# Kernel tuning notes

Measured on AMD Instinct MI355X. Metric: run time of the kernel, lower is better.

## Reference

```python
import jax, jax.numpy as jnp
import numpy as np

HEADS = 24
KV_HEADS = 6
HEAD_DIM = 64


def _partial_rope(x, cos, sin):
    # x: [B, H, S, head_dim]; cos/sin: [S, rot_dim]; rotate first rot_dim dims
    rot_dim = cos.shape[-1]
    x_rot, x_pass = x[..., :rot_dim], x[..., rot_dim:]
    half = rot_dim // 2
    # use_real_unbind_dim=-2: reshape (..., 2, half) then unbind -> first/second half
    x_real, x_imag = x_rot[..., :half], x_rot[..., half:]
    x_rotated = jnp.concatenate([-x_imag, x_real], axis=-1)
    out = x_rot * cos[None, None] + x_rotated * sin[None, None]
    return jnp.concatenate([out, x_pass], axis=-1)


def setup_inputs() -> dict:
    key = jax.random.key(0)
    ks = jax.random.split(key, 8)
    B, S, D = 2, 2048, 1536
    kv_dim = KV_HEADS * HEAD_DIM
    rot_dim = 32
    hidden_states = jax.random.normal(ks[0], (B, S, D), dtype=jnp.float32)
    # realistic rotary cos/sin from inv-freq angles
    pos = jnp.arange(S, dtype=jnp.float32)
    inv_freq = 1.0 / (10000.0 ** (jnp.arange(0, rot_dim, 2, dtype=jnp.float32) / rot_dim))
    ang = pos[:, None] * inv_freq[None, :]  # [S, rot_dim//2]
    ang = jnp.concatenate([ang, ang], axis=-1)  # [S, rot_dim]
    cos, sin = jnp.cos(ang), jnp.sin(ang)
    Wq = jax.random.normal(ks[1], (D, D), dtype=jnp.float32) * 0.02
    Wk = jax.random.normal(ks[2], (D, kv_dim), dtype=jnp.float32) * 0.02
    Wv = jax.random.normal(ks[3], (D, kv_dim), dtype=jnp.float32) * 0.02
    Wo = jax.random.normal(ks[4], (D, D), dtype=jnp.float32) * 0.02
    bo = jnp.zeros((D,), dtype=jnp.float32)
    return {"hidden_states": hidden_states, "cos": cos, "sin": sin,
            "Wq": Wq, "Wk": Wk, "Wv": Wv, "Wo": Wo, "bo": bo}


def reference(hidden_states, cos, sin, Wq, Wk, Wv, Wo, bo):
    B, S, D = hidden_states.shape
    residual = hidden_states
    q = hidden_states @ Wq  # [B,S,D]
    k = hidden_states @ Wk  # [B,S,kv_dim]
    v = hidden_states @ Wv
    q = q.reshape(B, S, HEADS, HEAD_DIM).transpose(0, 2, 1, 3)       # [B,H,S,d]
    k = k.reshape(B, S, KV_HEADS, HEAD_DIM).transpose(0, 2, 1, 3)    # [B,Hkv,S,d]
    v = v.reshape(B, S, KV_HEADS, HEAD_DIM).transpose(0, 2, 1, 3)
    rep = HEADS // KV_HEADS
    k = jnp.repeat(k, rep, axis=1)  # GQA repeat_interleave -> [B,H,S,d]
    v = jnp.repeat(v, rep, axis=1)
    # partial RoPE on query and key (self-attention)
    q = _partial_rope(q, cos, sin)
    k = _partial_rope(k, cos, sin)
    scale = 1.0 / jnp.sqrt(jnp.float32(HEAD_DIM))
    scores = jnp.einsum('bhqd,bhkd->bhqk', q, k) * scale
    probs = jax.nn.softmax(scores, axis=-1)
    out = jnp.einsum('bhqk,bhkd->bhqd', probs, v)
    out = out.transpose(0, 2, 1, 3).reshape(B, S, D)
    out = out @ Wo + bo
    return out + residual
```

## Files before the change

### kernel.cpp

```cpp
#include <hip/hip_runtime.h>

#define HEADS 24
#define KVH   6
#define HD    64
#define BB    2
#define SS    2048
#define DD    1536
#define KVD   384
#define NTOT  2304
#define MM    4096

typedef unsigned short ushort_t;
typedef __attribute__((ext_vector_type(8))) short short8;
typedef __attribute__((ext_vector_type(4))) float f32x4;

__device__ __forceinline__ ushort_t f2bf(float f) {
    union { float f; unsigned u; } v; v.f = f;
    return (ushort_t)((v.u + 0x8000u) >> 16);
}
__device__ __forceinline__ ushort_t f2bf_trunc(float f) {
    union { float f; unsigned u; } v; v.f = f;
    return (ushort_t)(v.u >> 16);
}
__device__ __forceinline__ unsigned pk2(float a, float b) {
    union { float f; unsigned u; } x, y; x.f = a; y.f = b;
    return ((x.u + 0x8000u) >> 16) | (((y.u + 0x8000u) >> 16) << 16);
}
#if __has_builtin(__builtin_amdgcn_exp2f)
#define EXP2(x) __builtin_amdgcn_exp2f(x)
#else
#define EXP2(x) exp2f(x)
#endif
__device__ __forceinline__ void glds16(const void* g, void* l) {
    __builtin_amdgcn_global_load_lds(
        (const __attribute__((address_space(1))) void*)g,
        (__attribute__((address_space(3))) void*)l, 16, 0, 0);
}

__device__ __forceinline__ void tconv_body(const float* __restrict__ in,
                                           ushort_t* __restrict__ out,
                                           int R, int C, int cb, int rb)
{
    __shared__ ushort_t tile[32][33];
    const int tx = threadIdx.x & 31, ty = threadIdx.x >> 5;
    const int c0 = cb * 32, r0 = rb * 32;
#pragma unroll
    for (int i = 0; i < 4; ++i)
        tile[ty + i * 8][tx] = f2bf(in[(size_t)(r0 + ty + i * 8) * C + c0 + tx]);
    __syncthreads();
#pragma unroll
    for (int i = 0; i < 4; ++i)
        out[(size_t)(c0 + ty + i * 8) * R + r0 + tx] = tile[tx][ty + i * 8];
}

#define NCVT (MM * DD / 4 / 256)
__global__ __launch_bounds__(256) void k_prep(const float* __restrict__ HS,
                                              const float* __restrict__ Wq,
                                              const float* __restrict__ Wk,
                                              const float* __restrict__ Wv,
                                              const float* __restrict__ Wo,
                                              ushort_t* __restrict__ Xbf,
                                              ushort_t* __restrict__ Wqt,
                                              ushort_t* __restrict__ Wkt,
                                              ushort_t* __restrict__ Wvt,
                                              ushort_t* __restrict__ Wot)
{
    int bid = blockIdx.x;
    if (bid < NCVT) {
        int i = bid * 256 + threadIdx.x;
        float4 v = ((const float4*)HS)[i];
        uint2 o = { pk2(v.x, v.y), pk2(v.z, v.w) };
        ((uint2*)Xbf)[i] = o;
        return;
    }
    bid -= NCVT;
    if (bid < 2304) { tconv_body(Wq, Wqt, DD, DD,  bid % 48, bid / 48); return; }
    bid -= 2304;
    if (bid < 576)  { tconv_body(Wk, Wkt, DD, KVD, bid % 12, bid / 12); return; }
    bid -= 576;
    if (bid < 576)  { tconv_body(Wv, Wvt, DD, KVD, bid % 12, bid / 12); return; }
    bid -= 576;
    tconv_body(Wo, Wot, DD, DD, bid % 48, bid / 48);
}

__global__ __launch_bounds__(256) void k_vt(const ushort_t* __restrict__ QKVb,
                                            ushort_t* __restrict__ VT)
{
    __shared__ ushort_t tile[32][33];
    const int tx = threadIdx.x & 31, ty = threadIdx.x >> 5;
    const int s0 = blockIdx.x * 32, c0 = blockIdx.y * 32, b = blockIdx.z;
#pragma unroll
    for (int i = 0; i < 4; ++i)
        tile[ty + i * 8][tx] =
            QKVb[(size_t)(b * SS + s0 + ty + i * 8) * NTOT + DD + KVD + c0 + tx];
    __syncthreads();
#pragma unroll
    for (int i = 0; i < 4; ++i)
        VT[((size_t)b * KVD + c0 + ty + i * 8) * SS + s0 + tx] = tile[tx][ty + i * 8];
}

__global__ __launch_bounds__(256) void k_qkv_mfma(const ushort_t* __restrict__ Xbf,
                                                  const ushort_t* __restrict__ Wqt,
                                                  const ushort_t* __restrict__ Wkt,
                                                  const ushort_t* __restrict__ Wvt,
                                                  const float* __restrict__ cosb,
                                                  const float* __restrict__ sinb,
                                                  ushort_t* __restrict__ QKVb)
{
    __shared__ ushort_t As[128][32];
    __shared__ ushort_t Bs[128][32];
    const int t = threadIdx.x, lane = t & 63, wave = t >> 6;
    const int n16 = lane & 15, quad = lane >> 4;
    const int wr = wave >> 1, wc = wave & 1;
    const int nt = blockIdx.x;
    const int n0 = nt * 128;
    const int m0 = blockIdx.y * 128;
    const ushort_t* Bt; int nl, mode;
    if (nt < 12)      { Bt = Wqt; nl = n0;            mode = 0; }
    else if (nt < 15) { Bt = Wkt; nl = n0 - DD;       mode = 1; }
    else              { Bt = Wvt; nl = n0 - DD - KVD; mode = 2; }

    const int srow = lane >> 2;
    const int scol = (lane & 3) * 8;
    const size_t aoff0 = (size_t)(m0 + wave * 16 + srow) * DD + scol;
    const size_t aoff1 = (size_t)(m0 + (wave + 4) * 16 + srow) * DD + scol;
    const size_t boff0 = (size_t)(nl + wave * 16 + srow) * DD + scol;
    const size_t boff1 = (size_t)(nl + (wave + 4) * 16 + srow) * DD + scol;
    ushort_t* lA0 = &As[wave * 16][0];
    ushort_t* lA1 = &As[(wave + 4) * 16][0];
    ushort_t* lB0 = &Bs[wave * 16][0];
    ushort_t* lB1 = &Bs[(wave + 4) * 16][0];

    f32x4 acc[4][4] = {};
    for (int k0 = 0; k0 < DD; k0 += 32) {
        __syncthreads();
        glds16(Xbf + aoff0 + k0, lA0);
        glds16(Xbf + aoff1 + k0, lA1);
        glds16(Bt  + boff0 + k0, lB0);
        glds16(Bt  + boff1 + k0, lB1);
        __syncthreads();
        short8 af[4], bf8[4];
#pragma unroll
        for (int i = 0; i < 4; ++i) af[i]  = *(const short8*)&As[wr * 64 + i * 16 + n16][quad * 8];
#pragma unroll
        for (int j = 0; j < 4; ++j) bf8[j] = *(const short8*)&Bs[wc * 64 + j * 16 + n16][quad * 8];
#pragma unroll
        for (int i = 0; i < 4; ++i)
#pragma unroll
            for (int j = 0; j < 4; ++j)
                acc[i][j] = __builtin_amdgcn_mfma_f32_16x16x32_bf16(af[i], bf8[j], acc[i][j], 0, 0, 0);
    }

    const float QSC = 0.18033688011112042f;
#pragma unroll
    for (int i = 0; i < 4; ++i) {
#pragma unroll
        for (int r = 0; r < 4; ++r) {
            const int row = m0 + wr * 64 + i * 16 + quad * 4 + r;
            ushort_t* outp = QKVb + (size_t)row * NTOT + n0 + wc * 64 + n16;
            float v0 = acc[i][0][r], v1 = acc[i][1][r];
            float v2 = acc[i][2][r], v3 = acc[i][3][r];
            if (mode < 2) {
                const int s = row & (SS - 1);
                float c0 = cosb[s * 32 + n16],      s0 = sinb[s * 32 + n16];
                float c1 = cosb[s * 32 + 16 + n16], s1 = sinb[s * 32 + 16 + n16];
                float nr = v0 * c0 - v1 * s0;
                float ni = v1 * c1 + v0 * s1;
                v0 = nr; v1 = ni;
            }
            if (mode == 0) { v0 *= QSC; v1 *= QSC; v2 *= QSC; v3 *= QSC; }
            outp[0]  = f2bf(v0);
            outp[16] = f2bf(v1);
            outp[32] = f2bf(v2);
            outp[48] = f2bf(v3);
        }
    }
}

__global__ __launch_bounds__(256) void k_attn(const ushort_t* __restrict__ QKVb,
                                              const ushort_t* __restrict__ VT,
                                              ushort_t* __restrict__ AOb)
{
    __shared__ __align__(16) ushort_t Ks[64][72];
    __shared__ __align__(16) ushort_t Vs[64][72];
    __shared__ __align__(16) ushort_t Ps[128][76];

    const int t    = threadIdx.x;
    const int wave = t >> 6;
    const int quad = (t >> 4) & 3;
    const int n16  = t & 15;
    const int q0   = blockIdx.x * 128;
    const int h    = blockIdx.y;
    const int b    = blockIdx.z;
    const int kh   = h >> 2;

    const int sr = t >> 2;
    const int sc = (t & 3) * 8;
    const int vc = (t & 3) * 16;

    short8 qf[2][2];
#pragma unroll
    for (int m = 0; m < 2; ++m)
#pragma unroll
        for (int kc = 0; kc < 2; ++kc)
            qf[m][kc] = *(const short8*)(QKVb +
                (size_t)(b * SS + q0 + wave * 32 + m * 16 + n16) * NTOT +
                h * HD + kc * 32 + quad * 8);

    float l_p[2][4] = {};
    f32x4 acc_o[2][4] = {};

    const ushort_t* Kbase = QKVb + (size_t)(b * SS) * NTOT + DD + kh * HD;
    const ushort_t* Vbase = VT + ((size_t)b * KVD + kh * 64) * SS;

    uint4 kp0, kp1, vp0, vp1;
    {
        const ushort_t* Kg = Kbase + (size_t)sr * NTOT + sc;
        kp0 = *(const uint4*)(Kg);
        kp1 = *(const uint4*)(Kg + 32);
        const ushort_t* Vg = Vbase + (size_t)sr * SS + vc;
        vp0 = *(const uint4*)(Vg);
        vp1 = *(const uint4*)(Vg + 8);
    }

    for (int kt = 0; kt < SS / 64; ++kt) {
        __syncthreads();
        *(uint4*)&Ks[sr][sc]      = kp0;
        *(uint4*)&Ks[sr][sc + 32] = kp1;
        *(uint4*)&Vs[sr][vc]      = vp0;
        *(uint4*)&Vs[sr][vc + 8]  = vp1;
        __syncthreads();

        if (kt + 1 < SS / 64) {
            const int k0n = (kt + 1) * 64;
            const ushort_t* Kg = Kbase + (size_t)(k0n + sr) * NTOT + sc;
            kp0 = *(const uint4*)(Kg);
            kp1 = *(const uint4*)(Kg + 32);
            const ushort_t* Vg = Vbase + (size_t)sr * SS + k0n + vc;
            vp0 = *(const uint4*)(Vg);
            vp1 = *(const uint4*)(Vg + 8);
        }

        f32x4 s_acc[2][4] = {};
#pragma unroll
        for (int kc = 0; kc < 2; ++kc) {
            short8 bf[4];
#pragma unroll
            for (int jj = 0; jj < 4; ++jj)
                bf[jj] = *(const short8*)&Ks[jj * 16 + n16][kc * 32 + quad * 8];
#pragma unroll
            for (int m = 0; m < 2; ++m)
#pragma unroll
                for (int jj = 0; jj < 4; ++jj)
                    s_acc[m][jj] = __builtin_amdgcn_mfma_f32_16x16x32_bf16(
                        qf[m][kc], bf[jj], s_acc[m][jj], 0, 0, 0);
        }

#pragma unroll
        for (int m = 0; m < 2; ++m)
#pragma unroll
            for (int r = 0; r < 4; ++r) {
                float p0 = EXP2(s_acc[m][0][r]);
                float p1 = EXP2(s_acc[m][1][r]);
                float p2 = EXP2(s_acc[m][2][r]);
                float p3 = EXP2(s_acc[m][3][r]);
                ushort_t* pr = &Ps[wave * 32 + m * 16 + quad * 4 + r][n16];
                pr[0]  = f2bf_trunc(p0);
                pr[16] = f2bf_trunc(p1);
                pr[32] = f2bf_trunc(p2);
                pr[48] = f2bf_trunc(p3);
                l_p[m][r] += (p0 + p1) + (p2 + p3);
            }

#pragma unroll
        for (int kc = 0; kc < 2; ++kc) {
            short8 vb[4];
#pragma unroll
            for (int dd = 0; dd < 4; ++dd)
                vb[dd] = *(const short8*)&Vs[dd * 16 + n16][kc * 32 + quad * 8];
#pragma unroll
            for (int m = 0; m < 2; ++m) {
                short8 pa = *(const short8*)&Ps[wave * 32 + m * 16 + n16][kc * 32 + quad * 8];
#pragma unroll
                for (int dd = 0; dd < 4; ++dd)
                    acc_o[m][dd] = __builtin_amdgcn_mfma_f32_16x16x32_bf16(
                        pa, vb[dd], acc_o[m][dd], 0, 0, 0);
            }
        }
    }

#pragma unroll
    for (int m = 0; m < 2; ++m) {
        float inv[4];
#pragma unroll
        for (int r = 0; r < 4; ++r) {
            float s = l_p[m][r];
#pragma unroll
            for (int msk = 1; msk < 16; msk <<= 1)
                s += __shfl_xor(s, msk);
            inv[r] = 1.0f / s;
        }
#pragma unroll
        for (int dd = 0; dd < 4; ++dd)
#pragma unroll
            for (int r = 0; r < 4; ++r) {
                int q = q0 + wave * 32 + m * 16 + quad * 4 + r;
                AOb[(size_t)(b * SS + q) * DD + h * HD + dd * 16 + n16] =
                    f2bf(acc_o[m][dd][r] * inv[r]);
            }
    }
}

__global__ __launch_bounds__(256) void k_out_mfma(const ushort_t* __restrict__ AOb,
                                                  const ushort_t* __restrict__ Wot,
                                                  const float* __restrict__ bo,
                                                  const float* __restrict__ HS,
                                                  float* __restrict__ out)
{
    __shared__ ushort_t As[128][32];
    __shared__ ushort_t Bs[128][32];
    const int t = threadIdx.x, lane = t & 63, wave = t >> 6;
    const int n16 = lane & 15, quad = lane >> 4;
    const int wr = wave >> 1, wc = wave & 1;
    const int n0 = blockIdx.x * 128;
    const int m0 = blockIdx.y * 128;

    const int srow = lane >> 2;
    const int scol = (lane & 3) * 8;
    const size_t aoff0 = (size_t)(m0 + wave * 16 + srow) * DD + scol;
    const size_t aoff1 = (size_t)(m0 + (wave + 4) * 16 + srow) * DD + scol;
    const size_t boff0 = (size_t)(n0 + wave * 16 + srow) * DD + scol;
    const size_t boff1 = (size_t)(n0 + (wave + 4) * 16 + srow) * DD + scol;
    ushort_t* lA0 = &As[wave * 16][0];
    ushort_t* lA1 = &As[(wave + 4) * 16][0];
    ushort_t* lB0 = &Bs[wave * 16][0];
    ushort_t* lB1 = &Bs[(wave + 4) * 16][0];

    f32x4 acc[4][4] = {};
    for (int k0 = 0; k0 < DD; k0 += 32) {
        __syncthreads();
        glds16(AOb + aoff0 + k0, lA0);
        glds16(AOb + aoff1 + k0, lA1);
        glds16(Wot + boff0 + k0, lB0);
        glds16(Wot + boff1 + k0, lB1);
        __syncthreads();
        short8 af[4], bf8[4];
#pragma unroll
        for (int i = 0; i < 4; ++i) af[i]  = *(const short8*)&As[wr * 64 + i * 16 + n16][quad * 8];
#pragma unroll
        for (int j = 0; j < 4; ++j) bf8[j] = *(const short8*)&Bs[wc * 64 + j * 16 + n16][quad * 8];
#pragma unroll
        for (int i = 0; i < 4; ++i)
#pragma unroll
            for (int j = 0; j < 4; ++j)
                acc[i][j] = __builtin_amdgcn_mfma_f32_16x16x32_bf16(af[i], bf8[j], acc[i][j], 0, 0, 0);
    }

    const int colb = n0 + wc * 64 + n16;
    float bo4[4];
#pragma unroll
    for (int j = 0; j < 4; ++j) bo4[j] = bo[colb + j * 16];
#pragma unroll
    for (int i = 0; i < 4; ++i) {
#pragma unroll
        for (int r = 0; r < 4; ++r) {
            const int row = m0 + wr * 64 + i * 16 + quad * 4 + r;
            float* op = out + (size_t)row * DD + colb;
            const float* hp = HS + (size_t)row * DD + colb;
#pragma unroll
            for (int j = 0; j < 4; ++j)
                op[j * 16] = acc[i][j][r] + bo4[j] + hp[j * 16];
        }
    }
}

extern "C" void kernel_launch(void* const* d_in, const int* in_sizes, int n_in,
                              void* d_out, int out_size, void* d_ws, size_t ws_size,
                              hipStream_t stream)
{
    const float* HS   = (const float*)d_in[0];
    const float* cosb = (const float*)d_in[1];
    const float* sinb = (const float*)d_in[2];
    const float* Wq   = (const float*)d_in[3];
    const float* Wk   = (const float*)d_in[4];
    const float* Wv   = (const float*)d_in[5];
    const float* Wo   = (const float*)d_in[6];
    const float* bo   = (const float*)d_in[7];
    float* out = (float*)d_out;

    ushort_t* Xbf  = (ushort_t*)d_ws;
    ushort_t* QKVb = Xbf  + (size_t)MM * DD;
    ushort_t* AOb  = QKVb + (size_t)MM * NTOT;
    ushort_t* Wqt  = AOb  + (size_t)MM * DD;
    ushort_t* Wkt  = Wqt  + (size_t)DD * DD;
    ushort_t* Wvt  = Wkt  + (size_t)KVD * DD;
    ushort_t* Wot  = Wvt  + (size_t)KVD * DD;
    ushort_t* VT   = Wot  + (size_t)DD * DD;

    const int nprep = NCVT + 2304 + 576 + 576 + 2304;
    k_prep    <<<dim3(nprep), 256, 0, stream>>>(HS, Wq, Wk, Wv, Wo,
                                                Xbf, Wqt, Wkt, Wvt, Wot);
    k_qkv_mfma<<<dim3(NTOT / 128, MM / 128), 256, 0, stream>>>(Xbf, Wqt, Wkt, Wvt, cosb, sinb, QKVb);
    k_vt      <<<dim3(SS / 32, KVD / 32, BB), 256, 0, stream>>>(QKVb, VT);
    k_attn    <<<dim3(SS / 128, HEADS, BB),   256, 0, stream>>>(QKVb, VT, AOb);
    k_out_mfma<<<dim3(DD / 128, MM / 128),    256, 0, stream>>>(AOb, Wot, bo, HS, out);
}
```

Before: 309.0 us.

## Compute V transposed directly via dedicated GEMM, drop transpose kernel

The V projection moves out of the fused QKV GEMM into a new kernel that computes Wv^T·X^T, so V is written already transposed and the separate k_vt transpose pass with its QKV round trip is removed. The QKV buffer shrinks to Q and K only. The output projection tile is halved in M (64x128) to launch more blocks. The attention K/V register prefetch is removed in favour of direct global-to-LDS loads each iteration, which may expose more load latency.

```diff
diff --git a/kernel.cpp b/kernel.cpp
--- a/kernel.cpp
+++ b/kernel.cpp
@@ -7,7 +7,7 @@
 #define SS    2048
 #define DD    1536
 #define KVD   384
-#define NTOT  2304
+#define QKD   1920
 #define MM    4096
 
 typedef unsigned short ushort_t;
@@ -83,26 +83,9 @@
     tconv_body(Wo, Wot, DD, DD, bid % 48, bid / 48);
 }
 
-__global__ __launch_bounds__(256) void k_vt(const ushort_t* __restrict__ QKVb,
-                                            ushort_t* __restrict__ VT)
-{
-    __shared__ ushort_t tile[32][33];
-    const int tx = threadIdx.x & 31, ty = threadIdx.x >> 5;
-    const int s0 = blockIdx.x * 32, c0 = blockIdx.y * 32, b = blockIdx.z;
-#pragma unroll
-    for (int i = 0; i < 4; ++i)
-        tile[ty + i * 8][tx] =
-            QKVb[(size_t)(b * SS + s0 + ty + i * 8) * NTOT + DD + KVD + c0 + tx];
-    __syncthreads();
-#pragma unroll
-    for (int i = 0; i < 4; ++i)
-        VT[((size_t)b * KVD + c0 + ty + i * 8) * SS + s0 + tx] = tile[tx][ty + i * 8];
-}
-
 __global__ __launch_bounds__(256) void k_qkv_mfma(const ushort_t* __restrict__ Xbf,
                                                   const ushort_t* __restrict__ Wqt,
                                                   const ushort_t* __restrict__ Wkt,
-                                                  const ushort_t* __restrict__ Wvt,
                                                   const float* __restrict__ cosb,
                                                   const float* __restrict__ sinb,
                                                   ushort_t* __restrict__ QKVb)
@@ -115,10 +98,9 @@
     const int nt = blockIdx.x;
     const int n0 = nt * 128;
     const int m0 = blockIdx.y * 128;
-    const ushort_t* Bt; int nl, mode;
-    if (nt < 12)      { Bt = Wqt; nl = n0;            mode = 0; }
-    else if (nt < 15) { Bt = Wkt; nl = n0 - DD;       mode = 1; }
-    else              { Bt = Wvt; nl = n0 - DD - KVD; mode = 2; }
+    const ushort_t* Bt; int nl, isq;
+    if (nt < 12) { Bt = Wqt; nl = n0;      isq = 1; }
+    else         { Bt = Wkt; nl = n0 - DD; isq = 0; }
 
     const int srow = lane >> 2;
     const int scol = (lane & 3) * 8;
@@ -157,10 +139,10 @@
 #pragma unroll
         for (int r = 0; r < 4; ++r) {
             const int row = m0 + wr * 64 + i * 16 + quad * 4 + r;
-            ushort_t* outp = QKVb + (size_t)row * NTOT + n0 + wc * 64 + n16;
+            ushort_t* outp = QKVb + (size_t)row * QKD + n0 + wc * 64 + n16;
             float v0 = acc[i][0][r], v1 = acc[i][1][r];
             float v2 = acc[i][2][r], v3 = acc[i][3][r];
-            if (mode < 2) {
+            {
                 const int s = row & (SS - 1);
                 float c0 = cosb[s * 32 + n16],      s0 = sinb[s * 32 + n16];
                 float c1 = cosb[s * 32 + 16 + n16], s1 = sinb[s * 32 + 16 + n16];
@@ -168,13 +150,66 @@
                 float ni = v1 * c1 + v0 * s1;
                 v0 = nr; v1 = ni;
             }
-            if (mode == 0) { v0 *= QSC; v1 *= QSC; v2 *= QSC; v3 *= QSC; }
+            if (isq) { v0 *= QSC; v1 *= QSC; v2 *= QSC; v3 *= QSC; }
             outp[0]  = f2bf(v0);
             outp[16] = f2bf(v1);
             outp[32] = f2bf(v2);
             outp[48] = f2bf(v3);
         }
     }
+}
+
+__global__ __launch_bounds__(256) void k_vtg(const ushort_t* __restrict__ Wvt,
+                                             const ushort_t* __restrict__ Xbf,
+                                             ushort_t* __restrict__ VT)
+{
+    __shared__ ushort_t As[64][32];
+    __shared__ ushort_t Bs[128][32];
+    const int t = threadIdx.x, lane = t & 63, wave = t >> 6;
+    const int n16 = lane & 15, quad = lane >> 4;
+    const int wr = wave >> 1, wc = wave & 1;
+    const int n0 = blockIdx.x * 128;
+    const int m0 = blockIdx.y * 64;
+
+    const int srow = lane >> 2;
+    const int scol = (lane & 3) * 8;
+    const size_t aoff  = (size_t)(m0 + wave * 16 + srow) * DD + scol;
+    const size_t boff0 = (size_t)(n0 + wave * 32 + srow) * DD + scol;
+    const size_t boff1 = boff0 + (size_t)16 * DD;
+    ushort_t* lA  = &As[wave * 16][0];
+    ushort_t* lB0 = &Bs[wave * 32][0];
+    ushort_t* lB1 = &Bs[wave * 32 + 16][0];
+
+    f32x4 acc[2][4] = {};
+    for (int k0 = 0; k0 < DD; k0 += 32) {
+        __syncthreads();
+        glds16(Wvt + aoff  + k0, lA);
+        glds16(Xbf + boff0 + k0, lB0);
+        glds16(Xbf + boff1 + k0, lB1);
+        __syncthreads();
+        short8 af[2], bf8[4];
+#pragma unroll
+        for (int i = 0; i < 2; ++i) af[i]  = *(const short8*)&As[wr * 32 + i * 16 + n16][quad * 8];
+#pragma unroll
+        for (int j = 0; j < 4; ++j) bf8[j] = *(const short8*)&Bs[wc * 64 + j * 16 + n16][quad * 8];
+#pragma unroll
+        for (int i = 0; i < 2; ++i)
+#pragma unroll
+            for (int j = 0; j < 4; ++j)
+                acc[i][j] = __builtin_amdgcn_mfma_f32_16x16x32_bf16(af[i], bf8[j], acc[i][j], 0, 0, 0);
+    }
+
+    const int b = n0 >> 11;
+#pragma unroll
+    for (int i = 0; i < 2; ++i)
+#pragma unroll
+        for (int r = 0; r < 4; ++r) {
+            const int c = m0 + wr * 32 + i * 16 + quad * 4 + r;
+            ushort_t* op = VT + ((size_t)b * KVD + c) * SS + (n0 & (SS - 1)) + wc * 64 + n16;
+#pragma unroll
+            for (int j = 0; j < 4; ++j)
+                op[j * 16] = f2bf(acc[i][j][r]);
+        }
 }
 
 __global__ __launch_bounds__(256) void k_attn(const ushort_t* __restrict__ QKVb,
@@ -204,42 +239,27 @@
 #pragma unroll
         for (int kc = 0; kc < 2; ++kc)
             qf[m][kc] = *(const short8*)(QKVb +
-                (size_t)(b * SS + q0 + wave * 32 + m * 16 + n16) * NTOT +
+                (size_t)(b * SS + q0 + wave * 32 + m * 16 + n16) * QKD +
                 h * HD + kc * 32 + quad * 8);
 
     float l_p[2][4] = {};
     f32x4 acc_o[2][4] = {};
 
-    const ushort_t* Kbase = QKVb + (size_t)(b * SS) * NTOT + DD + kh * HD;
+    const ushort_t* Kbase = QKVb + (size_t)(b * SS) * QKD + DD + kh * HD;
     const ushort_t* Vbase = VT + ((size_t)b * KVD + kh * 64) * SS;
 
-    uint4 kp0, kp1, vp0, vp1;
-    {
-        const ushort_t* Kg = Kbase + (size_t)sr * NTOT + sc;
-        kp0 = *(const uint4*)(Kg);
-        kp1 = *(const uint4*)(Kg + 32);
-        const ushort_t* Vg = Vbase + (size_t)sr * SS + vc;
-        vp0 = *(const uint4*)(Vg);
-        vp1 = *(const uint4*)(Vg + 8);
-    }
-
     for (int kt = 0; kt < SS / 64; ++kt) {
-        __syncthreads();
-        *(uint4*)&Ks[sr][sc]      = kp0;
-        *(uint4*)&Ks[sr][sc + 32] = kp1;
-        *(uint4*)&Vs[sr][vc]      = vp0;
-        *(uint4*)&Vs[sr][vc + 8]  = vp1;
-        __syncthreads();
-
-        if (kt + 1 < SS / 64) {
-            const int k0n = (kt + 1) * 64;
-            const ushort_t* Kg = Kbase + (size_t)(k0n + sr) * NTOT + sc;
-            kp0 = *(const uint4*)(Kg);
-            kp1 = *(const uint4*)(Kg + 32);
-            const ushort_t* Vg = Vbase + (size_t)sr * SS + k0n + vc;
-            vp0 = *(const uint4*)(Vg);
-            vp1 = *(const uint4*)(Vg + 8);
-        }
+        const int k0 = kt * 64;
+        __syncthreads();
+        {
+            const ushort_t* Kg = Kbase + (size_t)(k0 + sr) * QKD + sc;
+            *(uint4*)&Ks[sr][sc]      = *(const uint4*)(Kg);
+            *(uint4*)&Ks[sr][sc + 32] = *(const uint4*)(Kg + 32);
+            const ushort_t* Vg = Vbase + (size_t)sr * SS + k0 + vc;
+            *(uint4*)&Vs[sr][vc]      = *(const uint4*)(Vg);
+            *(uint4*)&Vs[sr][vc + 8]  = *(const uint4*)(Vg + 8);
+        }
+        __syncthreads();
 
         f32x4 s_acc[2][4] = {};
 #pragma unroll
@@ -317,40 +337,37 @@
                                                   const float* __restrict__ HS,
                                                   float* __restrict__ out)
 {
-    __shared__ ushort_t As[128][32];
+    __shared__ ushort_t As[64][32];
     __shared__ ushort_t Bs[128][32];
     const int t = threadIdx.x, lane = t & 63, wave = t >> 6;
     const int n16 = lane & 15, quad = lane >> 4;
     const int wr = wave >> 1, wc = wave & 1;
     const int n0 = blockIdx.x * 128;
-    const int m0 = blockIdx.y * 128;
+    const int m0 = blockIdx.y * 64;
 
     const int srow = lane >> 2;
     const int scol = (lane & 3) * 8;
-    const size_t aoff0 = (size_t)(m0 + wave * 16 + srow) * DD + scol;
-    const size_t aoff1 = (size_t)(m0 + (wave + 4) * 16 + srow) * DD + scol;
-    const size_t boff0 = (size_t)(n0 + wave * 16 + srow) * DD + scol;
-    const size_t boff1 = (size_t)(n0 + (wave + 4) * 16 + srow) * DD + scol;
-    ushort_t* lA0 = &As[wave * 16][0];
-    ushort_t* lA1 = &As[(wave + 4) * 16][0];
-    ushort_t* lB0 = &Bs[wave * 16][0];
-    ushort_t* lB1 = &Bs[(wave + 4) * 16][0];
-
-    f32x4 acc[4][4] = {};
+    const size_t aoff  = (size_t)(m0 + wave * 16 + srow) * DD + scol;
+    const size_t boff0 = (size_t)(n0 + wave * 32 + srow) * DD + scol;
+    const size_t boff1 = boff0 + (size_t)16 * DD;
+    ushort_t* lA  = &As[wave * 16][0];
+    ushort_t* lB0 = &Bs[wave * 32][0];
+    ushort_t* lB1 = &Bs[wave * 32 + 16][0];
+
+    f32x4 acc[2][4] = {};
     for (int k0 = 0; k0 < DD; k0 += 32) {
         __syncthreads();
-        glds16(AOb + aoff0 + k0, lA0);
-        glds16(AOb + aoff1 + k0, lA1);
+        glds16(AOb + aoff  + k0, lA);
         glds16(Wot + boff0 + k0, lB0);
         glds16(Wot + boff1 + k0, lB1);
         __syncthreads();
-        short8 af[4], bf8[4];
-#pragma unroll
-        for (int i = 0; i < 4; ++i) af[i]  = *(const short8*)&As[wr * 64 + i * 16 + n16][quad * 8];
+        short8 af[2], bf8[4];
+#pragma unroll
+        for (int i = 0; i < 2; ++i) af[i]  = *(const short8*)&As[wr * 32 + i * 16 + n16][quad * 8];
 #pragma unroll
         for (int j = 0; j < 4; ++j) bf8[j] = *(const short8*)&Bs[wc * 64 + j * 16 + n16][quad * 8];
 #pragma unroll
-        for (int i = 0; i < 4; ++i)
+        for (int i = 0; i < 2; ++i)
 #pragma unroll
             for (int j = 0; j < 4; ++j)
                 acc[i][j] = __builtin_amdgcn_mfma_f32_16x16x32_bf16(af[i], bf8[j], acc[i][j], 0, 0, 0);
@@ -361,10 +378,10 @@
 #pragma unroll
     for (int j = 0; j < 4; ++j) bo4[j] = bo[colb + j * 16];
 #pragma unroll
-    for (int i = 0; i < 4; ++i) {
+    for (int i = 0; i < 2; ++i) {
 #pragma unroll
         for (int r = 0; r < 4; ++r) {
-            const int row = m0 + wr * 64 + i * 16 + quad * 4 + r;
+            const int row = m0 + wr * 32 + i * 16 + quad * 4 + r;
             float* op = out + (size_t)row * DD + colb;
             const float* hp = HS + (size_t)row * DD + colb;
 #pragma unroll
@@ -390,7 +407,7 @@
 
     ushort_t* Xbf  = (ushort_t*)d_ws;
     ushort_t* QKVb = Xbf  + (size_t)MM * DD;
-    ushort_t* AOb  = QKVb + (size_t)MM * NTOT;
+    ushort_t* AOb  = QKVb + (size_t)MM * QKD;
     ushort_t* Wqt  = AOb  + (size_t)MM * DD;
     ushort_t* Wkt  = Wqt  + (size_t)DD * DD;
     ushort_t* Wvt  = Wkt  + (size_t)KVD * DD;
@@ -400,8 +417,8 @@
     const int nprep = NCVT + 2304 + 576 + 576 + 2304;
     k_prep    <<<dim3(nprep), 256, 0, stream>>>(HS, Wq, Wk, Wv, Wo,
                                                 Xbf, Wqt, Wkt, Wvt, Wot);
-    k_qkv_mfma<<<dim3(NTOT / 128, MM / 128), 256, 0, stream>>>(Xbf, Wqt, Wkt, Wvt, cosb, sinb, QKVb);
-    k_vt      <<<dim3(SS / 32, KVD / 32, BB), 256, 0, stream>>>(QKVb, VT);
-    k_attn    <<<dim3(SS / 128, HEADS, BB),   256, 0, stream>>>(QKVb, VT, AOb);
-    k_out_mfma<<<dim3(DD / 128, MM / 128),    256, 0, stream>>>(AOb, Wot, bo, HS, out);
-}
+    k_qkv_mfma<<<dim3(QKD / 128, MM / 128), 256, 0, stream>>>(Xbf, Wqt, Wkt, cosb, sinb, QKVb);
+    k_vtg     <<<dim3(MM / 128, KVD / 64),  256, 0, stream>>>(Wvt, Xbf, VT);
+    k_attn    <<<dim3(SS / 128, HEADS, BB), 256, 0, stream>>>(QKVb, VT, AOb);
+    k_out_mfma<<<dim3(DD / 128, MM / 64),   256, 0, stream>>>(AOb, Wot, bo, HS, out);
+}
```

After: 288.2 us. 6.7% less time.
